# Performance work log

Hardware: AMD Instinct MI355X
Metric: run time of the kernel (lower is better)

Reference implementation:

```python
import jax, jax.numpy as jnp
import numpy as np

N_SUPPORT = 8192
N_QUERY = 8192
INPUT_DIM = 1024
EMBED_DIM = 512
N_CLASSES = 64


def setup_inputs() -> dict:
    key = jax.random.key(0)
    k1, k2, k3, k4 = jax.random.split(key, 4)
    support_data = jax.random.normal(k1, (N_SUPPORT, INPUT_DIM), dtype=jnp.float32)
    query_data = jax.random.normal(k2, (N_QUERY, INPUT_DIM), dtype=jnp.float32)
    support_labels = jax.random.randint(k3, (N_SUPPORT,), 0, N_CLASSES, dtype=jnp.int32)
    W = jax.random.normal(k4, (INPUT_DIM, EMBED_DIM), dtype=jnp.float32) * (1.0 / np.sqrt(INPUT_DIM))
    return {"support_data": support_data, "support_labels": support_labels,
            "query_data": query_data, "W": W}


def _l2_normalize(x, eps=1e-12):
    # Matches F.normalize(p=2): x / max(||x||, eps)
    n = jnp.linalg.norm(x, axis=-1, keepdims=True)
    return x / jnp.maximum(n, eps)


def reference(support_data, support_labels, query_data, W):
    # encoder: single linear projection
    s_emb = support_data @ W            # [Ns, D]
    q_emb = query_data @ W              # [Nq, D]
    s_norm = _l2_normalize(s_emb)
    q_norm = _l2_normalize(q_emb)
    # cosine similarities for all query/support pairs: [Nq, Ns]
    sims = q_norm @ s_norm.T
    # per-class sum over support samples (torch.unique -> sorted 0..N_CLASSES-1)
    # segment_sum along the support axis: [N_classes, Nq] -> [Nq, N_classes]
    class_scores = jax.ops.segment_sum(sims.T, support_labels, num_segments=N_CLASSES).T
    return jax.nn.softmax(class_scores, axis=-1)
```

## Files before the change

kernel.cpp:

```cpp
#include <hip/hip_runtime.h>
#include <hip/hip_bf16.h>

#define NS 8192
#define NQ 8192
#define NTOT 16384
#define KDIM 1024
#define ED 512
#define NC 64
#define PBLK 64

typedef __attribute__((ext_vector_type(4))) float fx4;
typedef __attribute__((ext_vector_type(4))) int ix4;
typedef __attribute__((ext_vector_type(8))) short sx8;
typedef __attribute__((ext_vector_type(4))) unsigned short ux4;
typedef __attribute__((ext_vector_type(8))) unsigned short ux8;

__device__ __forceinline__ unsigned short f2bf(float f) {
  union { float f; unsigned u; } v; v.f = f;
  unsigned r = v.u + 0x7fffu + ((v.u >> 16) & 1u);
  return (unsigned short)(r >> 16);
}
__device__ __forceinline__ float bf2f(unsigned short h) {
  union { unsigned u; float f; } v; v.u = ((unsigned)h) << 16;
  return v.f;
}

__device__ __forceinline__ void async_ld16(const void* g, void* l) {
  __builtin_amdgcn_global_load_lds(
      (const __attribute__((address_space(1))) unsigned int*)g,
      (__attribute__((address_space(3))) unsigned int*)l, 16, 0, 0);
}

__global__ __launch_bounds__(256) void k_prep(
    const float* __restrict__ W, unsigned short* __restrict__ Wt,
    float* __restrict__ rowssq) {
  __shared__ float tile[32][33];
  int bid = blockIdx.x;
  int t = threadIdx.x;
  int k0 = (bid & 31) * 32;
  int n0 = (bid >> 5) * 32;
  int tx = t & 31, ty = t >> 5;
#pragma unroll
  for (int i = ty; i < 32; i += 8)
    tile[i][tx] = W[(size_t)(k0 + i) * ED + n0 + tx];
  __syncthreads();
#pragma unroll
  for (int i = ty; i < 32; i += 8)
    Wt[(size_t)(n0 + i) * KDIM + k0 + tx] = f2bf(tile[tx][i]);
  if (t < 32) rowssq[bid * 32 + t] = 0.f;
}

__global__ __launch_bounds__(256) void k_gemm_embed(
    const float* __restrict__ Xs, const float* __restrict__ Xq,
    const unsigned short* __restrict__ Wt,
    unsigned short* __restrict__ emb, float* __restrict__ rowssq) {
  __shared__ unsigned short Ash[2][128 * 8 * 8];
  __shared__ unsigned short Bsh[2][128 * 8 * 8];

  int lid = blockIdx.x;
  int x = lid & 7;
  int s = lid >> 3;
  int m_blk = x * 16 + (s >> 2);
  int n_blk = s & 3;

  const float* Xsrc = (m_blk < 64)
      ? (Xs + (size_t)m_blk * 128 * KDIM)
      : (Xq + (size_t)(m_blk - 64) * 128 * KDIM);
  const unsigned short* Wrow = Wt + (size_t)n_blk * 128 * KDIM;

  int t = threadIdx.x;
  int lane = t & 63, w = t >> 6;
  int wm = w >> 1, wn = w & 1;
  int quad = lane >> 4, ml = lane & 15;

  fx4 acc[4][4];
#pragma unroll
  for (int i = 0; i < 4; ++i)
#pragma unroll
    for (int j = 0; j < 4; ++j) acc[i][j] = fx4{0.f, 0.f, 0.f, 0.f};

  fx4 av[4][2];

  auto loadA = [&](int kt) {
    int k0 = kt * 64;
#pragma unroll
    for (int c = 0; c < 4; ++c) {
      int ch = t + 256 * c;
      int m = ch >> 3, kq = ch & 7;
      const float* g = &Xsrc[(size_t)m * KDIM + k0 + kq * 8];
      av[c][0] = *(const fx4*)g;
      av[c][1] = *(const fx4*)(g + 4);
    }
  };
  auto writeA = [&](int b) {
#pragma unroll
    for (int c = 0; c < 4; ++c) {
      int ch = t + 256 * c;
      int m = ch >> 3, kq = ch & 7;
      ux8 o;
      o[0] = f2bf(av[c][0].x); o[1] = f2bf(av[c][0].y);
      o[2] = f2bf(av[c][0].z); o[3] = f2bf(av[c][0].w);
      o[4] = f2bf(av[c][1].x); o[5] = f2bf(av[c][1].y);
      o[6] = f2bf(av[c][1].z); o[7] = f2bf(av[c][1].w);
      *(ux8*)&Ash[b][((m * 8) + (kq ^ (m & 7))) * 8] = o;
    }
  };
  auto stageB = [&](int kt, int b) {
    int k0 = kt * 64;
#pragma unroll
    for (int c = 0; c < 4; ++c) {
      int ch = t + 256 * c;
      int n = ch >> 3;
      int kq = (ch & 7) ^ (n & 7);
      async_ld16(&Wrow[(size_t)n * KDIM + k0 + kq * 8],
                 &Bsh[b][(w * 64 + 256 * c) * 8]);
    }
  };

  loadA(0);
  stageB(0, 0);
  writeA(0);
  for (int kt = 0; kt < 16; ++kt) {
    int b = kt & 1;
    __syncthreads();
    if (kt < 15) { loadA(kt + 1); stageB(kt + 1, b ^ 1); }
#pragma unroll
    for (int s2 = 0; s2 < 2; ++s2) {
      int kq = s2 * 4 + quad;
      sx8 af[4], bfr[4];
#pragma unroll
      for (int i = 0; i < 4; ++i) {
        int row = wm * 64 + i * 16 + ml;
        af[i] = *(const sx8*)&Ash[b][(row * 8 + (kq ^ (row & 7))) * 8];
      }
#pragma unroll
      for (int j = 0; j < 4; ++j) {
        int nrow = wn * 64 + j * 16 + ml;
        bfr[j] = *(const sx8*)&Bsh[b][(nrow * 8 + (kq ^ (nrow & 7))) * 8];
      }
#pragma unroll
      for (int i = 0; i < 4; ++i)
#pragma unroll
        for (int j = 0; j < 4; ++j)
          acc[i][j] = __builtin_amdgcn_mfma_f32_16x16x32_bf16(af[i], bfr[j], acc[i][j], 0, 0, 0);
    }
    if (kt < 15) writeA(b ^ 1);
  }

  int grow = m_blk * 128 + wm * 64;
  int gcol = n_blk * 128 + wn * 64;
#pragma unroll
  for (int i = 0; i < 4; ++i) {
#pragma unroll
    for (int r = 0; r < 4; ++r) {
      int mrow = grow + i * 16 + quad * 4 + r;
      float p = 0.f;
#pragma unroll
      for (int j = 0; j < 4; ++j) {
        emb[(size_t)mrow * ED + gcol + j * 16 + ml] = f2bf(acc[i][j][r]);
        p += acc[i][j][r] * acc[i][j][r];
      }
#pragma unroll
      for (int off = 1; off < 16; off <<= 1) p += __shfl_xor(p, off, 16);
      if (ml == 0) atomicAdd(&rowssq[mrow], p);
    }
  }
}

__global__ __launch_bounds__(256) void k_proto_partial(
    const unsigned short* __restrict__ embS, const float* __restrict__ rowssq,
    const int* __restrict__ labels, float* __restrict__ Ppart) {
  __shared__ float Pl[NC * 64];
  int t = threadIdx.x;
#pragma unroll
  for (int i = 0; i < 16; ++i) Pl[i * 256 + t] = 0.f;
  __syncthreads();

  int w = t >> 6, lane = t & 63;
  int ds = blockIdx.y;
  int row0 = blockIdx.x * (NS / PBLK);
#pragma unroll 4
  for (int r = w; r < NS / PBLK; r += 4) {
    int row = row0 + r;
    int lbl = labels[row];
    float scale = 1.0f / fmaxf(sqrtf(rowssq[row]), 1e-12f);
    float v = bf2f(embS[(size_t)row * ED + ds * 64 + lane]) * scale;
    atomicAdd(&Pl[lbl * 64 + lane], v);
  }
  __syncthreads();

  float* o = Ppart + (size_t)blockIdx.x * NC * ED + ds * 64;
#pragma unroll
  for (int i = 0; i < 16; ++i) {
    int idx = i * 256 + t;
    o[(size_t)(idx >> 6) * ED + (idx & 63)] = Pl[idx];
  }
}

__global__ __launch_bounds__(256) void k_proto_reduce(
    const float* __restrict__ Ppart, unsigned short* __restrict__ Pbf) {
  int idx = blockIdx.x * 256 + threadIdx.x;
  int kq = idx >> 9;
  int n = (idx >> 3) & 63;
  int j = idx & 7;
  int d = kq * 8 + j;
  float s = 0.f;
#pragma unroll 8
  for (int b = 0; b < PBLK; ++b) s += Ppart[(size_t)b * NC * ED + n * ED + d];
  Pbf[idx] = f2bf(s);
}

__global__ __launch_bounds__(64) void k_scores(
    const unsigned short* __restrict__ embQ, const float* __restrict__ ssqQ,
    const unsigned short* __restrict__ Pbf, float* __restrict__ out) {
  int lane = threadIdx.x;
  int quad = lane >> 4, ml = lane & 15;
  int qrow0 = blockIdx.x * 16;

  fx4 acc[4];
#pragma unroll
  for (int i = 0; i < 4; ++i) acc[i] = fx4{0.f, 0.f, 0.f, 0.f};

#pragma unroll 4
  for (int ki = 0; ki < 16; ++ki) {
    sx8 a = *(const sx8*)&embQ[(size_t)(qrow0 + ml) * ED + ki * 32 + quad * 8];
#pragma unroll
    for (int nt = 0; nt < 4; ++nt) {
      sx8 b = *(const sx8*)&Pbf[((ki * 4 + quad) * 64 + nt * 16 + ml) * 8];
      acc[nt] = __builtin_amdgcn_mfma_f32_16x16x32_bf16(a, b, acc[nt], 0, 0, 0);
    }
  }

#pragma unroll
  for (int r = 0; r < 4; ++r) {
    int qq = qrow0 + quad * 4 + r;
    float scale = 1.0f / fmaxf(sqrtf(ssqQ[qq]), 1e-12f);
    float s[4];
#pragma unroll
    for (int nt = 0; nt < 4; ++nt) s[nt] = acc[nt][r] * scale;
    float m = fmaxf(fmaxf(s[0], s[1]), fmaxf(s[2], s[3]));
#pragma unroll
    for (int off = 1; off < 16; off <<= 1) m = fmaxf(m, __shfl_xor(m, off, 16));
    float e[4], ssum = 0.f;
#pragma unroll
    for (int nt = 0; nt < 4; ++nt) { e[nt] = __expf(s[nt] - m); ssum += e[nt]; }
#pragma unroll
    for (int off = 1; off < 16; off <<= 1) ssum += __shfl_xor(ssum, off, 16);
    float inv = 1.0f / ssum;
#pragma unroll
    for (int nt = 0; nt < 4; ++nt)
      out[(size_t)qq * NC + nt * 16 + ml] = e[nt] * inv;
  }
}

extern "C" void kernel_launch(void* const* d_in, const int* in_sizes, int n_in,
                              void* d_out, int out_size, void* d_ws, size_t ws_size,
                              hipStream_t stream) {
  const float* Xs     = (const float*)d_in[0];
  const int*   labels = (const int*)d_in[1];
  const float* Xq     = (const float*)d_in[2];
  const float* W      = (const float*)d_in[3];
  float* out = (float*)d_out;

  char* ws = (char*)d_ws;
  size_t off = 0;
  unsigned short* Wt  = (unsigned short*)(ws + off); off += (size_t)ED * KDIM * 2;
  unsigned short* emb = (unsigned short*)(ws + off); off += (size_t)NTOT * ED * 2;
  float* rowssq = (float*)(ws + off); off += (size_t)NTOT * 4;
  float* Ppart  = (float*)(ws + off); off += (size_t)PBLK * NC * ED * 4;
  unsigned short* Pbf = (unsigned short*)(ws + off); off += (size_t)NC * ED * 2;

  k_prep<<<512, 256, 0, stream>>>(W, Wt, rowssq);
  k_gemm_embed<<<512, 256, 0, stream>>>(Xs, Xq, Wt, emb, rowssq);
  k_proto_partial<<<dim3(PBLK, 8), 256, 0, stream>>>(emb, rowssq, labels, Ppart);
  k_proto_reduce<<<NC * ED / 256, 256, 0, stream>>>(Ppart, Pbf);
  k_scores<<<NQ / 16, 64, 0, stream>>>(emb + (size_t)NS * ED, rowssq + NS, Pbf, out);
}
```

Before: 181.3 us.

## Deepen A-tile register prefetch to two stages with explicit waitcnt barriers

In the projection GEMM, the fp32 A tiles are now prefetched two k-steps ahead into a double-buffered register array, instead of one. `__syncthreads` is replaced by a raw `s_barrier` preceded by `s_waitcnt vmcnt(8)`, so the newest A loads stay in flight across the barrier. `sched_barrier` and `s_setprio` around the MFMA block control instruction ordering and wave priority. The aim is to hide global load latency behind the MFMAs, at the cost of about 32 more VGPRs (which may lower occupancy) and redundant loads of the last tile near the end of the loop.

```diff
diff --git a/kernel.cpp b/kernel.cpp
--- a/kernel.cpp
+++ b/kernel.cpp
@@ -79,29 +79,29 @@
 #pragma unroll
     for (int j = 0; j < 4; ++j) acc[i][j] = fx4{0.f, 0.f, 0.f, 0.f};
 
-  fx4 av[4][2];
-
-  auto loadA = [&](int kt) {
+  fx4 av[2][4][2];
+
+  auto loadA = [&](int kt, int slot) {
     int k0 = kt * 64;
 #pragma unroll
     for (int c = 0; c < 4; ++c) {
       int ch = t + 256 * c;
       int m = ch >> 3, kq = ch & 7;
       const float* g = &Xsrc[(size_t)m * KDIM + k0 + kq * 8];
-      av[c][0] = *(const fx4*)g;
-      av[c][1] = *(const fx4*)(g + 4);
+      av[slot][c][0] = *(const fx4*)g;
+      av[slot][c][1] = *(const fx4*)(g + 4);
     }
   };
-  auto writeA = [&](int b) {
+  auto writeA = [&](int slot, int b) {
 #pragma unroll
     for (int c = 0; c < 4; ++c) {
       int ch = t + 256 * c;
       int m = ch >> 3, kq = ch & 7;
       ux8 o;
-      o[0] = f2bf(av[c][0].x); o[1] = f2bf(av[c][0].y);
-      o[2] = f2bf(av[c][0].z); o[3] = f2bf(av[c][0].w);
-      o[4] = f2bf(av[c][1].x); o[5] = f2bf(av[c][1].y);
-      o[6] = f2bf(av[c][1].z); o[7] = f2bf(av[c][1].w);
+      o[0] = f2bf(av[slot][c][0].x); o[1] = f2bf(av[slot][c][0].y);
+      o[2] = f2bf(av[slot][c][0].z); o[3] = f2bf(av[slot][c][0].w);
+      o[4] = f2bf(av[slot][c][1].x); o[5] = f2bf(av[slot][c][1].y);
+      o[6] = f2bf(av[slot][c][1].z); o[7] = f2bf(av[slot][c][1].w);
       *(ux8*)&Ash[b][((m * 8) + (kq ^ (m & 7))) * 8] = o;
     }
   };
@@ -117,13 +117,23 @@
     }
   };
 
-  loadA(0);
   stageB(0, 0);
-  writeA(0);
+  __builtin_amdgcn_sched_barrier(0);
+  loadA(0, 0);
+  loadA(1, 1);
+  __builtin_amdgcn_sched_barrier(0);
+  writeA(0, 0);
+  asm volatile("s_waitcnt vmcnt(8) lgkmcnt(0)" ::: "memory");
+  __builtin_amdgcn_sched_barrier(0);
+  __builtin_amdgcn_s_barrier();
+
   for (int kt = 0; kt < 16; ++kt) {
     int b = kt & 1;
-    __syncthreads();
-    if (kt < 15) { loadA(kt + 1); stageB(kt + 1, b ^ 1); }
+    stageB(kt + 1 < 16 ? kt + 1 : 15, b ^ 1);
+    __builtin_amdgcn_sched_barrier(0);
+    loadA(kt + 2 < 16 ? kt + 2 : 15, b);
+
+    __builtin_amdgcn_s_setprio(1);
 #pragma unroll
     for (int s2 = 0; s2 < 2; ++s2) {
       int kq = s2 * 4 + quad;
@@ -144,7 +154,12 @@
         for (int j = 0; j < 4; ++j)
           acc[i][j] = __builtin_amdgcn_mfma_f32_16x16x32_bf16(af[i], bfr[j], acc[i][j], 0, 0, 0);
     }
-    if (kt < 15) writeA(b ^ 1);
+    __builtin_amdgcn_s_setprio(0);
+
+    writeA(b ^ 1, b ^ 1);
+    asm volatile("s_waitcnt vmcnt(8) lgkmcnt(0)" ::: "memory");
+    __builtin_amdgcn_sched_barrier(0);
+    __builtin_amdgcn_s_barrier();
   }
 
   int grow = m_blk * 128 + wm * 64;
```

New measurement: 264.7 us. 1.46x slower.

## Deepen projection GEMM pipeline with double register prefetch and manual waitcnt scheduling

Applied to the files above, without the earlier changes.

Rewrites the main loop of the projection GEMM so the A tiles for two k-steps are prefetched into alternating register sets. The loop is unrolled by two with explicit sched_barriers, s_waitcnt vmcnt(8) and s_barrier instead of __syncthreads. This lets global loads for future tiles stay in flight across the MFMA compute, and compute is wrapped in s_setprio to favour the matrix work. The cost is more registers, redundant clamped loads at the tail, and fragile hand-tuned wait counts.

```diff
diff --git a/kernel.cpp b/kernel.cpp
--- a/kernel.cpp
+++ b/kernel.cpp
@@ -79,9 +79,9 @@
 #pragma unroll
     for (int j = 0; j < 4; ++j) acc[i][j] = fx4{0.f, 0.f, 0.f, 0.f};
 
-  fx4 av[4][2];
-
-  auto loadA = [&](int kt) {
+  fx4 avA[4][2], avB[4][2];
+
+  auto loadA = [&](int kt, fx4 (&av)[4][2]) {
     int k0 = kt * 64;
 #pragma unroll
     for (int c = 0; c < 4; ++c) {
@@ -92,7 +92,7 @@
       av[c][1] = *(const fx4*)(g + 4);
     }
   };
-  auto writeA = [&](int b) {
+  auto writeA = [&](const fx4 (&av)[4][2], int bbuf) {
 #pragma unroll
     for (int c = 0; c < 4; ++c) {
       int ch = t + 256 * c;
@@ -102,7 +102,7 @@
       o[2] = f2bf(av[c][0].z); o[3] = f2bf(av[c][0].w);
       o[4] = f2bf(av[c][1].x); o[5] = f2bf(av[c][1].y);
       o[6] = f2bf(av[c][1].z); o[7] = f2bf(av[c][1].w);
-      *(ux8*)&Ash[b][((m * 8) + (kq ^ (m & 7))) * 8] = o;
+      *(ux8*)&Ash[bbuf][((m * 8) + (kq ^ (m & 7))) * 8] = o;
     }
   };
   auto stageB = [&](int kt, int b) {
@@ -116,14 +116,7 @@
                  &Bsh[b][(w * 64 + 256 * c) * 8]);
     }
   };
-
-  loadA(0);
-  stageB(0, 0);
-  writeA(0);
-  for (int kt = 0; kt < 16; ++kt) {
-    int b = kt & 1;
-    __syncthreads();
-    if (kt < 15) { loadA(kt + 1); stageB(kt + 1, b ^ 1); }
+  auto compute = [&](int b) {
 #pragma unroll
     for (int s2 = 0; s2 < 2; ++s2) {
       int kq = s2 * 4 + quad;
@@ -144,7 +137,45 @@
         for (int j = 0; j < 4; ++j)
           acc[i][j] = __builtin_amdgcn_mfma_f32_16x16x32_bf16(af[i], bfr[j], acc[i][j], 0, 0, 0);
     }
-    if (kt < 15) writeA(b ^ 1);
+  };
+
+  stageB(0, 0);
+  __builtin_amdgcn_sched_barrier(0);
+  loadA(0, avA);
+  loadA(1, avB);
+  __builtin_amdgcn_sched_barrier(0);
+  writeA(avA, 0);
+  asm volatile("s_waitcnt vmcnt(8) lgkmcnt(0)" ::: "memory");
+  __builtin_amdgcn_sched_barrier(0);
+  __builtin_amdgcn_s_barrier();
+
+  for (int it = 0; it < 8; ++it) {
+    int kt0 = it * 2;
+    stageB(kt0 + 1, 1);
+    __builtin_amdgcn_sched_barrier(0);
+    loadA(kt0 + 2 < 16 ? kt0 + 2 : 15, avA);
+
+    __builtin_amdgcn_s_setprio(1);
+    compute(0);
+    __builtin_amdgcn_s_setprio(0);
+
+    writeA(avB, 1);
+    asm volatile("s_waitcnt vmcnt(8) lgkmcnt(0)" ::: "memory");
+    __builtin_amdgcn_sched_barrier(0);
+    __builtin_amdgcn_s_barrier();
+
+    stageB(kt0 + 2 < 16 ? kt0 + 2 : 15, 0);
+    __builtin_amdgcn_sched_barrier(0);
+    loadA(kt0 + 3 < 16 ? kt0 + 3 : 15, avB);
+
+    __builtin_amdgcn_s_setprio(1);
+    compute(1);
+    __builtin_amdgcn_s_setprio(0);
+
+    writeA(avA, 0);
+    asm volatile("s_waitcnt vmcnt(8) lgkmcnt(0)" ::: "memory");
+    __builtin_amdgcn_sched_barrier(0);
+    __builtin_amdgcn_s_barrier();
   }
 
   int grow = m_blk * 128 + wm * 64;
```

After: 177.3 us. 2.2% less time.
